# Performance work log

Hardware: AMD Instinct MI355X
Metric: run time of the kernel (lower is better)

Reference implementation:

```python
import math
import jax, jax.numpy as jnp
import numpy as np

NUM_TOKENS = 8192
MODEL_DIM = 4096
NUM_EXPERTS = 64
CAPACITY_FACTOR = 1.0


def setup_inputs() -> dict:
    key = jax.random.key(0)
    k1, k2 = jax.random.split(key)
    x = jax.random.normal(k1, (NUM_TOKENS, MODEL_DIM), dtype=jnp.float32)
    wg = jax.random.normal(k2, (NUM_EXPERTS, MODEL_DIM), dtype=jnp.float32) * 0.02
    return {"x": x, "wg": wg}


def reference(x, wg):
    # gate projection: nn.Linear(model_dim, num_experts, bias=False)
    logits = jnp.einsum("td,ed->te", x, wg)  # [T, E]
    T, E = logits.shape
    capacity = int(CAPACITY_FACTOR * math.ceil(T / E))  # train mode

    gates = jax.nn.softmax(logits, axis=1)  # [T, E]
    indices1_s = jnp.argmax(gates, axis=1)  # [T]
    mask1 = jax.nn.one_hot(indices1_s, E, dtype=jnp.int32)  # [T, E]

    # gate value of the selected expert (before capacity dropping)
    gates1_s = jnp.sum(gates * mask1.astype(gates.dtype), axis=1)  # [T]

    # position of each token within its expert's queue
    locations1 = jnp.cumsum(mask1, axis=0) - 1  # [T, E]

    # load-balancing auxiliary loss
    me = jnp.mean(gates, axis=0)
    ce = jnp.mean(mask1.astype(gates.dtype), axis=0)
    l_aux = jnp.mean(me * ce) * (E * E)

    # drop tokens beyond expert capacity
    mask1 = mask1 * (locations1 < capacity).astype(mask1.dtype)
    locations1_s = jnp.sum(locations1 * mask1, axis=1)  # [T]

    gates1 = gates1_s[:, None] * mask1.astype(gates1_s.dtype)  # [T, E]
    locations1_sc = jax.nn.one_hot(locations1_s, capacity, dtype=gates1.dtype)  # [T, C]
    # combine1_sec = bmm(gates1[:, :, None], locations1_sc[:, None, :])
    combine1_sec = gates1[:, :, None] * locations1_sc[:, None, :]  # [T, E, C]
    dispatch_mask = combine1_sec != 0
    return (l_aux, combine1_sec, dispatch_mask)
```

## Files before the change

### kernel.cpp

```cpp
#include <hip/hip_runtime.h>
#include <hip/hip_bf16.h>
#include <cstdint>
#include <cstddef>

#define T_TOK 8192
#define MDIM  4096
#define NEXP  64
#define CAP   128
#define TEC   ((size_t)T_TOK * NEXP * CAP)
#define OUTN  ((size_t)(1 + 2 * TEC))

typedef __attribute__((ext_vector_type(8))) short bf16x8;
typedef __attribute__((ext_vector_type(4))) float f32x4;

__device__ __forceinline__ void split8(const float* f, bf16x8& h, bf16x8& l) {
#pragma unroll
  for (int j = 0; j < 8; ++j) {
    const __hip_bfloat16 hb = __float2bfloat16(f[j]);
    const float r = f[j] - __bfloat162float(hb);
    h[j] = __builtin_bit_cast(short, hb);
    l[j] = __builtin_bit_cast(short, __float2bfloat16(r));
  }
}

__device__ __forceinline__ void gll16(const void* g, void* l) {
  __builtin_amdgcn_global_load_lds(
      (const __attribute__((address_space(1))) void*)g,
      (__attribute__((address_space(3))) void*)l, 16, 0, 0);
}

template <int N>
__device__ __forceinline__ void vwait() {
  if constexpr (N == 0)      asm volatile("s_waitcnt vmcnt(0) lgkmcnt(0)" ::: "memory");
  else if constexpr (N == 1) asm volatile("s_waitcnt vmcnt(1) lgkmcnt(0)" ::: "memory");
  else                       asm volatile("s_waitcnt vmcnt(2) lgkmcnt(0)" ::: "memory");
}
__device__ __forceinline__ void barrier_now() {
  __builtin_amdgcn_s_barrier();
  asm volatile("" ::: "memory");
}

__global__ __launch_bounds__(256) void wsplit(
    const float* __restrict__ wg, short* __restrict__ wh,
    short* __restrict__ wl, float* __restrict__ esum) {
  const int i = blockIdx.x * 256 + threadIdx.x;
  const float4 v = ((const float4*)wg)[i];
  const float a[4] = {v.x, v.y, v.z, v.w};
  short4 h, l;
  short* hp = &h.x; short* lp = &l.x;
#pragma unroll
  for (int j = 0; j < 4; ++j) {
    const __hip_bfloat16 hb = __float2bfloat16(a[j]);
    const float r = a[j] - __bfloat162float(hb);
    hp[j] = __builtin_bit_cast(short, hb);
    lp[j] = __builtin_bit_cast(short, __float2bfloat16(r));
  }
  ((short4*)wh)[i] = h;
  ((short4*)wl)[i] = l;
  if (blockIdx.x == 0 && threadIdx.x < NEXP) esum[threadIdx.x] = 0.f;
}

__global__ __launch_bounds__(1024, 8) void gemm_fill_softmax(
    const float* __restrict__ x, const short* __restrict__ wh,
    const short* __restrict__ wl, int* __restrict__ idx,
    float* __restrict__ gval, float* __restrict__ esum,
    float* __restrict__ out) {
  __shared__ __align__(16) char LDS[73728];
  const int tid = threadIdx.x;
  const int bid = blockIdx.x;

  if (bid >= 256) {
    const int f = bid - 256;
    f32x4* o4 = (f32x4*)out;
    const f32x4 zv = {0.f, 0.f, 0.f, 0.f};
    size_t g = (size_t)f * 131072 + tid;
#pragma unroll 4
    for (int i = 0; i < 128; ++i) {
      __builtin_nontemporal_store(zv, o4 + g);
      g += 1024;
    }
    if (f == 0 && tid == 0) out[OUTN - 1] = 0.f;
    return;
  }

  const int t0 = bid * 32;

  const int wid  = tid >> 6;
  const int lane = tid & 63;
  const int tt   = wid & 1;
  const int et   = (wid >> 1) & 3;
  const int kc   = wid >> 3;
  const int mrow = lane & 15;
  const int kg   = lane >> 4;

  const int spl  = tid >> 9;
  const int su   = tid & 511;
  const int sexp = su >> 3;
  const int sq   = su & 7;
  const int sm   = sq ^ (sexp & 7);
  const short* bsrc0 = (spl ? wl : wh) + (size_t)sexp * MDIM +
                       (sm >> 2) * 2048 + (sm & 3) * 8;
  const int atok = tid >> 4;
  const int as   = tid & 15;
  const int apr  = (as >> 1) ^ (atok & 7);
  const float* asrc0 = x + (size_t)(t0 + atok) * MDIM +
                       (apr >> 2) * 2048 + (apr & 3) * 8 + (as & 1) * 4;

  const int w8 = __builtin_amdgcn_readfirstlane((tid >> 9) == 0 ? 1 : 0);

  const int tok   = tt * 16 + mrow;
  const int abyte = tok * 256 + (((kc * 4 + kg) ^ (tok & 7)) << 5);
  const int expi  = et * 16 + mrow;
  const int bbyte = expi * 128 + (((kc * 4 + kg) ^ (expi & 7)) << 4);

  f32x4 acc = {0.f, 0.f, 0.f, 0.f};

  auto stage = [&](int j, int buf) {
    const int b = buf * 8192;
    gll16(bsrc0 + j * 32, LDS + 24576 + spl * 24576 + b + su * 16);
    if (w8) gll16(asrc0 + j * 32, LDS + b + (tid << 4));
  };
  auto compute = [&](int kb, int buf) {
    const int b = buf * 8192;
    const char* ab = LDS + b;
    const f32x4 a0 = *(const f32x4*)(ab + abyte);
    const f32x4 a1 = *(const f32x4*)(ab + abyte + 16);
    const float fa[8] = {a0[0], a0[1], a0[2], a0[3], a1[0], a1[1], a1[2], a1[3]};
    bf16x8 ah, al;
    split8(fa, ah, al);
    const bf16x8 bhv = *(const bf16x8*)(LDS + 24576 + b + bbyte);
    const bf16x8 blv = *(const bf16x8*)(LDS + 49152 + b + bbyte);
    acc = __builtin_amdgcn_mfma_f32_16x16x32_bf16(ah, bhv, acc, 0, 0, 0);
    acc = __builtin_amdgcn_mfma_f32_16x16x32_bf16(ah, blv, acc, 0, 0, 0);
    acc = __builtin_amdgcn_mfma_f32_16x16x32_bf16(al, bhv, acc, 0, 0, 0);
  };

  stage(0, 0); stage(1, 1);

  int cb = 0, sb = 2;
#pragma unroll 3
  for (int kb = 0; kb < 62; ++kb) {
    if (w8) vwait<2>(); else vwait<1>();
    barrier_now();
    stage(kb + 2, sb);
    compute(kb, cb);
    cb = (cb == 2) ? 0 : cb + 1;
    sb = (sb == 2) ? 0 : sb + 1;
  }
  if (w8) vwait<2>(); else vwait<1>();
  barrier_now(); compute(62, 2);
  vwait<0>();
  barrier_now(); compute(63, 0);

  __syncthreads();

  float* redF = (float*)LDS;
#pragma unroll
  for (int r = 0; r < 4; ++r)
    redF[(kc * 32 + tt * 16 + kg * 4 + r) * 64 + et * 16 + mrow] = acc[r];
  __syncthreads();

  float gl = 0.f;
#pragma unroll
  for (int j = 0; j < 2; ++j) {
    const int tk = wid * 2 + j;
    const float v = redF[tk * 64 + lane] + redF[(32 + tk) * 64 + lane];
    float m = v; int mi = lane;
#pragma unroll
    for (int d = 32; d >= 1; d >>= 1) {
      const float om = __shfl_xor(m, d);
      const int   oi = __shfl_xor(mi, d);
      if (om > m || (om == m && oi < mi)) { m = om; mi = oi; }
    }
    const float e = expf(v - m);
    float denom = e;
#pragma unroll
    for (int d = 32; d >= 1; d >>= 1) denom += __shfl_xor(denom, d);
    gl += e / denom;
    if (lane == 0) { idx[t0 + tk] = mi; gval[t0 + tk] = 1.0f / denom; }
  }

  float* sgF = (float*)(LDS + 16384);
  sgF[wid * 64 + lane] = gl;
  __syncthreads();
  if (tid < 64) {
    float s = 0.f;
#pragma unroll
    for (int w = 0; w < 16; ++w) s += sgF[w * 64 + tid];
    atomicAdd(&esum[tid], s);
  }
}

__global__ __launch_bounds__(256) void scan_scatter(
    const int* __restrict__ idx, const float* __restrict__ gval,
    const float* __restrict__ esum, float* __restrict__ out) {
  __shared__ int sidx[T_TOK];
  const int tid = threadIdx.x;
  for (int i = tid; i < T_TOK / 4; i += 256)
    ((int4*)sidx)[i] = ((const int4*)idx)[i];
  __syncthreads();

  const int e    = blockIdx.x * 4 + (tid >> 6);
  const int lane = tid & 63;
  int carry = 0;
#pragma unroll 4
  for (int base = 0; base < T_TOK; base += 64) {
    const int t = base + lane;
    const bool flag = (sidx[t] == e);
    const unsigned long long mask = __ballot(flag);
    if (flag) {
      const int p = carry + __popcll(mask & ((1ull << lane) - 1ull));
      if (p < CAP) {
        const size_t off = ((size_t)t * NEXP + e) * CAP + p;
        out[1 + off]       = gval[t];
        out[1 + TEC + off] = 1.0f;
      }
    }
    carry += __popcll(mask);
  }
  if (lane == 0)
    atomicAdd(out, esum[e] * (float)carry *
                   ((float)NEXP / ((float)T_TOK * (float)T_TOK)));
}

extern "C" void kernel_launch(void* const* d_in, const int* in_sizes, int n_in,
                              void* d_out, int out_size, void* d_ws, size_t ws_size,
                              hipStream_t stream) {
  const float* x  = (const float*)d_in[0];
  const float* wg = (const float*)d_in[1];
  float* out = (float*)d_out;

  short* wh   = (short*)d_ws;
  short* wl   = wh + (size_t)NEXP * MDIM;
  int*   idx  = (int*)(wl + (size_t)NEXP * MDIM);
  float* gval = (float*)(idx + T_TOK);
  float* esum = (float*)(gval + T_TOK);

  wsplit<<<(NEXP * MDIM / 4) / 256, 256, 0, stream>>>(wg, wh, wl, esum);
  gemm_fill_softmax<<<512, 1024, 0, stream>>>(x, wh, wl, idx, gval, esum, out);
  scan_scatter<<<NEXP / 4, 256, 0, stream>>>(idx, gval, esum, out);
}
```

Measured before the change: 139.9 us.

## Fuse scan-scatter into GEMM kernel with atomic-counter cross-block synchronization

Removes the separate scan_scatter launch. Its work now runs on 16 trailing blocks of the fused kernel, which spin-wait on global done and fill counters before scattering. The zero-fill is redistributed: GEMM blocks fill a slice after finishing, filler blocks take the remainder, and the scatter blocks fill a small share before waiting. This hides the launch gap and overlaps the scatter with the tail of the fill, at the cost of relying on co-residency of all 512 blocks to avoid deadlock.

```diff
diff --git a/kernel.cpp b/kernel.cpp
--- a/kernel.cpp
+++ b/kernel.cpp
@@ -42,7 +42,7 @@
 
 __global__ __launch_bounds__(256) void wsplit(
     const float* __restrict__ wg, short* __restrict__ wh,
-    short* __restrict__ wl, float* __restrict__ esum) {
+    short* __restrict__ wl, float* __restrict__ esum, int* __restrict__ cnts) {
   const int i = blockIdx.x * 256 + threadIdx.x;
   const float4 v = ((const float4*)wg)[i];
   const float a[4] = {v.x, v.y, v.z, v.w};
@@ -58,28 +58,87 @@
   ((short4*)wh)[i] = h;
   ((short4*)wl)[i] = l;
   if (blockIdx.x == 0 && threadIdx.x < NEXP) esum[threadIdx.x] = 0.f;
-}
-
-__global__ __launch_bounds__(1024, 8) void gemm_fill_softmax(
+  if (blockIdx.x == 0 && threadIdx.x < 2)   cnts[threadIdx.x] = 0;
+}
+
+__global__ __launch_bounds__(1024, 8) void fused(
     const float* __restrict__ x, const short* __restrict__ wh,
     const short* __restrict__ wl, int* __restrict__ idx,
     float* __restrict__ gval, float* __restrict__ esum,
-    float* __restrict__ out) {
+    int* __restrict__ cnts, float* __restrict__ out) {
   __shared__ __align__(16) char LDS[73728];
   const int tid = threadIdx.x;
   const int bid = blockIdx.x;
-
-  if (bid >= 256) {
-    const int f = bid - 256;
-    f32x4* o4 = (f32x4*)out;
-    const f32x4 zv = {0.f, 0.f, 0.f, 0.f};
-    size_t g = (size_t)f * 131072 + tid;
+  int* donecnt = cnts;
+  int* fillcnt = cnts + 1;
+
+  const f32x4 zv = {0.f, 0.f, 0.f, 0.f};
+  f32x4* o4 = (f32x4*)out;
+
+  auto ntfill = [&](long long startUnit, int iters) {
+    size_t g = (size_t)startUnit * 4096 + tid;
 #pragma unroll 4
-    for (int i = 0; i < 128; ++i) {
+    for (int i = 0; i < iters; ++i) {
       __builtin_nontemporal_store(zv, o4 + g);
       g += 1024;
     }
-    if (f == 0 && tid == 0) out[OUTN - 1] = 0.f;
+  };
+  auto signal = [&](int* cnt) {
+    asm volatile("s_waitcnt vmcnt(0) lgkmcnt(0)" ::: "memory");
+    __threadfence();
+    __syncthreads();
+    if (tid == 0) atomicAdd(cnt, 1);
+  };
+  auto spin = [&](int* cnt, int target) {
+    if (tid == 0) {
+      while (__hip_atomic_load(cnt, __ATOMIC_ACQUIRE,
+                               __HIP_MEMORY_SCOPE_AGENT) < target)
+        __builtin_amdgcn_s_sleep(8);
+    }
+    __syncthreads();
+  };
+
+  if (bid >= 256) {
+    if (bid < 496) {
+      ntfill(1536LL + (long long)(bid - 256) * 27, 108);
+      signal(fillcnt);
+      return;
+    }
+    const int s = bid - 496;
+    ntfill(8016LL + (long long)s * 11, 44);
+    signal(fillcnt);
+
+    spin(donecnt, 256);
+    int* sidx = (int*)LDS;
+    for (int i = tid; i < T_TOK / 4; i += 1024)
+      ((int4*)sidx)[i] = ((const int4*)idx)[i];
+    __syncthreads();
+    spin(fillcnt, 512);
+
+    const int wid  = tid >> 6;
+    const int lane = tid & 63;
+    if (wid < 4) {
+      const int e = s * 4 + wid;
+      int carry = 0;
+#pragma unroll 4
+      for (int base = 0; base < T_TOK; base += 64) {
+        const int t = base + lane;
+        const bool flag = (sidx[t] == e);
+        const unsigned long long mask = __ballot(flag);
+        if (flag) {
+          const int p = carry + __popcll(mask & ((1ull << lane) - 1ull));
+          if (p < CAP) {
+            const size_t off = ((size_t)t * NEXP + e) * CAP + p;
+            out[1 + off]       = gval[t];
+            out[1 + TEC + off] = 1.0f;
+          }
+        }
+        carry += __popcll(mask);
+      }
+      if (lane == 0)
+        atomicAdd(out, esum[e] * (float)carry *
+                       ((float)NEXP / ((float)T_TOK * (float)T_TOK)));
+    }
     return;
   }
 
@@ -189,38 +248,12 @@
     for (int w = 0; w < 16; ++w) s += sgF[w * 64 + tid];
     atomicAdd(&esum[tid], s);
   }
-}
-
-__global__ __launch_bounds__(256) void scan_scatter(
-    const int* __restrict__ idx, const float* __restrict__ gval,
-    const float* __restrict__ esum, float* __restrict__ out) {
-  __shared__ int sidx[T_TOK];
-  const int tid = threadIdx.x;
-  for (int i = tid; i < T_TOK / 4; i += 256)
-    ((int4*)sidx)[i] = ((const int4*)idx)[i];
-  __syncthreads();
-
-  const int e    = blockIdx.x * 4 + (tid >> 6);
-  const int lane = tid & 63;
-  int carry = 0;
-#pragma unroll 4
-  for (int base = 0; base < T_TOK; base += 64) {
-    const int t = base + lane;
-    const bool flag = (sidx[t] == e);
-    const unsigned long long mask = __ballot(flag);
-    if (flag) {
-      const int p = carry + __popcll(mask & ((1ull << lane) - 1ull));
-      if (p < CAP) {
-        const size_t off = ((size_t)t * NEXP + e) * CAP + p;
-        out[1 + off]       = gval[t];
-        out[1 + TEC + off] = 1.0f;
-      }
-    }
-    carry += __popcll(mask);
-  }
-  if (lane == 0)
-    atomicAdd(out, esum[e] * (float)carry *
-                   ((float)NEXP / ((float)T_TOK * (float)T_TOK)));
+
+  signal(donecnt);
+
+  ntfill((long long)bid * 6, 24);
+  if (bid == 0 && tid == 0) out[OUTN - 1] = 0.f;
+  signal(fillcnt);
 }
 
 extern "C" void kernel_launch(void* const* d_in, const int* in_sizes, int n_in,
@@ -235,8 +268,8 @@
   int*   idx  = (int*)(wl + (size_t)NEXP * MDIM);
   float* gval = (float*)(idx + T_TOK);
   float* esum = (float*)(gval + T_TOK);
-
-  wsplit<<<(NEXP * MDIM / 4) / 256, 256, 0, stream>>>(wg, wh, wl, esum);
-  gemm_fill_softmax<<<512, 1024, 0, stream>>>(x, wh, wl, idx, gval, esum, out);
-  scan_scatter<<<NEXP / 4, 256, 0, stream>>>(idx, gval, esum, out);
-}
+  int*   cnts = (int*)(esum + NEXP);
+
+  wsplit<<<(NEXP * MDIM / 4) / 256, 256, 0, stream>>>(wg, wh, wl, esum, cnts);
+  fused<<<512, 1024, 0, stream>>>(x, wh, wl, idx, gval, esum, cnts, out);
+}
```

After: 500.3 us. 258% more time.
